# Kernel tuning notes

Measured on AMD Instinct MI355X. Metric: run time of the kernel, lower is better.

## Reference

```python
import jax, jax.numpy as jnp
import numpy as np

B, T, D = 8, 2048, 1024
FF = 4 * D
EPS = 1e-5


def setup_inputs() -> dict:
    key = jax.random.key(0)
    ks = jax.random.split(key, 20)
    rn = lambda k, s, sc=0.02: (jax.random.normal(k, s, jnp.float32) * sc)
    return {
        "x": jax.random.normal(ks[0], (B, T, D), jnp.float32),
        "ln1_g": jnp.ones((D,), jnp.float32),
        "ln1_b": jnp.zeros((D,), jnp.float32),
        "ln2_g": jnp.ones((D,), jnp.float32),
        "ln2_b": jnp.zeros((D,), jnp.float32),
        # time-mixing lerp coefficients in [0,1]
        "tm_mix_k": jax.random.uniform(ks[1], (D,), jnp.float32),
        "tm_mix_v": jax.random.uniform(ks[2], (D,), jnp.float32),
        "tm_mix_r": jax.random.uniform(ks[3], (D,), jnp.float32),
        # per-channel decay (log-log space, w = -exp(time_decay)) and first-token bonus
        "time_decay": rn(ks[4], (D,), 1.0),
        "time_first": rn(ks[5], (D,), 0.5),
        "wk": rn(ks[6], (D, D)),
        "wv": rn(ks[7], (D, D)),
        "wr": rn(ks[8], (D, D)),
        "wo": rn(ks[9], (D, D)),
        "cm_mix_k": jax.random.uniform(ks[10], (D,), jnp.float32),
        "cm_mix_r": jax.random.uniform(ks[11], (D,), jnp.float32),
        "cwk": rn(ks[12], (D, FF)),
        "cwv": rn(ks[13], (FF, D)),
        "cwr": rn(ks[14], (D, D)),
    }


def layer_norm(x, g, b):
    mu = jnp.mean(x, axis=-1, keepdims=True)
    var = jnp.var(x, axis=-1, keepdims=True)
    return (x - mu) * jax.lax.rsqrt(var + EPS) * g + b


def token_shift(x):
    # x[:, t-1] with zeros at t=0 (fresh state)
    return jnp.pad(x, ((0, 0), (1, 0), (0, 0)))[:, :-1]


def wkv_scan(k, v, time_decay, time_first):
    """Numerically-stable RWKV-4 WKV linear recurrence. k,v: [B,T,D]."""
    w = -jnp.exp(time_decay)  # [D], negative log-decay per step
    u = time_first

    def step(carry, kv):
        aa, bb, pp = carry  # each [B, D]
        kt, vt = kv
        ww = u + kt
        p = jnp.maximum(pp, ww)
        e1 = jnp.exp(pp - p)
        e2 = jnp.exp(ww - p)
        out = (e1 * aa + e2 * vt) / (e1 * bb + e2)
        ww2 = pp + w
        p2 = jnp.maximum(ww2, kt)
        e1b = jnp.exp(ww2 - p2)
        e2b = jnp.exp(kt - p2)
        return (e1b * aa + e2b * vt, e1b * bb + e2b, p2), out

    z = jnp.zeros((k.shape[0], k.shape[2]), k.dtype)
    init = (z, z, jnp.full_like(z, -1e38))
    _, outs = jax.lax.scan(step, init, (jnp.moveaxis(k, 1, 0), jnp.moveaxis(v, 1, 0)))
    return jnp.moveaxis(outs, 0, 1)  # [B,T,D]


def reference(x, ln1_g, ln1_b, ln2_g, ln2_b,
              tm_mix_k, tm_mix_v, tm_mix_r, time_decay, time_first,
              wk, wv, wr, wo, cm_mix_k, cm_mix_r, cwk, cwv, cwr):
    # --- Time mixing (pre-LN residual) ---
    h = layer_norm(x, ln1_g, ln1_b)
    hx = token_shift(h)
    k = jnp.einsum("btd,de->bte", h * tm_mix_k + hx * (1.0 - tm_mix_k), wk)
    v = jnp.einsum("btd,de->bte", h * tm_mix_v + hx * (1.0 - tm_mix_v), wv)
    r = jax.nn.sigmoid(jnp.einsum("btd,de->bte", h * tm_mix_r + hx * (1.0 - tm_mix_r), wr))
    wkv = wkv_scan(k, v, time_decay, time_first)
    x = x + jnp.einsum("btd,de->bte", r * wkv, wo)

    # --- Channel mixing (pre-LN residual) ---
    h = layer_norm(x, ln2_g, ln2_b)
    hx = token_shift(h)
    kk = jnp.einsum("btd,df->btf", h * cm_mix_k + hx * (1.0 - cm_mix_k), cwk)
    kk = jnp.square(jax.nn.relu(kk))  # [B,T,4D]
    rr = jax.nn.sigmoid(jnp.einsum("btd,de->bte", h * cm_mix_r + hx * (1.0 - cm_mix_r), cwr))
    x = x + rr * jnp.einsum("btf,fd->btd", kk, cwv)
    return x
```

## Files before the change

kernel.cpp:

```cpp
#include <hip/hip_runtime.h>

typedef unsigned short u16;
typedef float f32x4 __attribute__((ext_vector_type(4)));
typedef __bf16 bf16x8 __attribute__((ext_vector_type(8)));
typedef u16 u16x8 __attribute__((ext_vector_type(8)));
typedef u16 u16x4 __attribute__((ext_vector_type(4)));

static constexpr int D  = 1024;
static constexpr int T  = 2048;
static constexpr int NB = 8;
static constexpr int M  = NB * T;
static constexpr int FF = 4096;
static constexpr int NCH = 32;
static constexpr int CL  = T / NCH;

__device__ __forceinline__ u16 f2bf(float f) {
  unsigned u = __builtin_bit_cast(unsigned, f);
  return (u16)((u + 0x7fffu + ((u >> 16) & 1u)) >> 16);
}
__device__ __forceinline__ float bf2f(u16 s) {
  return __builtin_bit_cast(float, (unsigned)s << 16);
}

__device__ __forceinline__ void gload16(const u16* g, u16* l) {
  __builtin_amdgcn_global_load_lds(
      (const __attribute__((address_space(1))) void*)g,
      (__attribute__((address_space(3))) void*)l, 16, 0, 0);
}

__global__ __launch_bounds__(256) void ln_kernel(const float* __restrict__ x,
                                                 const float* __restrict__ g,
                                                 const float* __restrict__ b,
                                                 u16* __restrict__ h) {
  __shared__ float red[8];
  const int m = blockIdx.x;
  const int tid = threadIdx.x;
  const float* xr = x + (size_t)m * D;
  f32x4 v = *(const f32x4*)&xr[tid * 4];
  float s  = v[0] + v[1] + v[2] + v[3];
  float s2 = v[0]*v[0] + v[1]*v[1] + v[2]*v[2] + v[3]*v[3];
  #pragma unroll
  for (int o = 32; o > 0; o >>= 1) { s += __shfl_down(s, o); s2 += __shfl_down(s2, o); }
  if ((tid & 63) == 0) { red[tid >> 6] = s; red[4 + (tid >> 6)] = s2; }
  __syncthreads();
  s  = red[0] + red[1] + red[2] + red[3];
  s2 = red[4] + red[5] + red[6] + red[7];
  const float mu = s * (1.0f / D);
  const float rs = rsqrtf(s2 * (1.0f / D) - mu * mu + 1e-5f);
  u16x4 o4;
  #pragma unroll
  for (int i = 0; i < 4; ++i) {
    int d = tid * 4 + i;
    o4[i] = f2bf((v[i] - mu) * rs * g[d] + b[d]);
  }
  *(u16x4*)&h[(size_t)m * D + tid * 4] = o4;
}

__global__ __launch_bounds__(256) void mix3_kernel(const u16* __restrict__ h,
    const float* __restrict__ mk, const float* __restrict__ mv, const float* __restrict__ mr,
    u16* __restrict__ xk, u16* __restrict__ xv, u16* __restrict__ xr) {
  const int m = blockIdx.x;
  const int tid = threadIdx.x;
  const size_t base = (size_t)m * D + tid * 4;
  u16x4 hv = *(const u16x4*)&h[base];
  u16x4 hp = {0, 0, 0, 0};
  if ((m % T) != 0) hp = *(const u16x4*)&h[base - D];
  u16x4 ok, ov, orr;
  #pragma unroll
  for (int i = 0; i < 4; ++i) {
    int d = tid * 4 + i;
    float hc = bf2f(hv[i]), hx = bf2f(hp[i]);
    float a;
    a = mk[d]; ok[i]  = f2bf(hc * a + hx * (1.0f - a));
    a = mv[d]; ov[i]  = f2bf(hc * a + hx * (1.0f - a));
    a = mr[d]; orr[i] = f2bf(hc * a + hx * (1.0f - a));
  }
  *(u16x4*)&xk[base] = ok;
  *(u16x4*)&xv[base] = ov;
  *(u16x4*)&xr[base] = orr;
}

__global__ __launch_bounds__(256) void mix2_kernel(const u16* __restrict__ h,
    const float* __restrict__ mk, const float* __restrict__ mr,
    u16* __restrict__ xk, u16* __restrict__ xr) {
  const int m = blockIdx.x;
  const int tid = threadIdx.x;
  const size_t base = (size_t)m * D + tid * 4;
  u16x4 hv = *(const u16x4*)&h[base];
  u16x4 hp = {0, 0, 0, 0};
  if ((m % T) != 0) hp = *(const u16x4*)&h[base - D];
  u16x4 ok, orr;
  #pragma unroll
  for (int i = 0; i < 4; ++i) {
    int d = tid * 4 + i;
    float hc = bf2f(hv[i]), hx = bf2f(hp[i]);
    float a;
    a = mk[d]; ok[i]  = f2bf(hc * a + hx * (1.0f - a));
    a = mr[d]; orr[i] = f2bf(hc * a + hx * (1.0f - a));
  }
  *(u16x4*)&xk[base] = ok;
  *(u16x4*)&xr[base] = orr;
}

__global__ __launch_bounds__(256) void transpose_bf16_kernel(const float* __restrict__ in,
                                                             u16* __restrict__ out,
                                                             int K_, int N_) {
  __shared__ u16 t[32][33];
  const int k0 = blockIdx.x * 32, n0 = blockIdx.y * 32;
  const int r = threadIdx.x >> 5, c = threadIdx.x & 31;
  #pragma unroll
  for (int p = 0; p < 4; ++p)
    t[r + p * 8][c] = f2bf(in[(size_t)(k0 + r + p * 8) * N_ + n0 + c]);
  __syncthreads();
  #pragma unroll
  for (int p = 0; p < 4; ++p)
    out[(size_t)(n0 + r + p * 8) * K_ + k0 + c] = t[c][r + p * 8];
}

__global__ __launch_bounds__(256) void wkv_phase1(const float* __restrict__ K_,
                                                  const u16* __restrict__ V_,
                                                  const float* __restrict__ td,
                                                  float* __restrict__ aggA,
                                                  float* __restrict__ aggB,
                                                  float* __restrict__ aggP) {
  const int gid = blockIdx.x * 256 + threadIdx.x;
  const int d = gid & (D - 1);
  const int c = (gid >> 10) & (NCH - 1);
  const int b = gid >> 15;
  const float w = -expf(td[d]);
  float a = 0.0f, bb = 0.0f, p = -1e38f;
  size_t idx = ((size_t)b * T + (size_t)c * CL) * D + d;
  for (int t = 0; t < CL; ++t, idx += D) {
    const float kt = K_[idx];
    const float vt = bf2f(V_[idx]);
    const float wp = p + w;
    const float pn = fmaxf(wp, kt);
    const float e1 = expf(wp - pn), e2 = expf(kt - pn);
    a  = e1 * a  + e2 * vt;
    bb = e1 * bb + e2;
    p  = pn;
  }
  aggA[gid] = a; aggB[gid] = bb; aggP[gid] = p;
}

__global__ __launch_bounds__(256) void wkv_phase2(const float* __restrict__ td,
                                                  const float* __restrict__ aggA,
                                                  const float* __restrict__ aggB,
                                                  const float* __restrict__ aggP,
                                                  float* __restrict__ incA,
                                                  float* __restrict__ incB,
                                                  float* __restrict__ incP) {
  const int gid = blockIdx.x * 256 + threadIdx.x;
  const int d = gid & (D - 1);
  const int b = gid >> 10;
  const float cw = -expf(td[d]) * (float)CL;
  float a = 0.0f, bb = 0.0f, p = -1e38f;
  for (int c = 0; c < NCH; ++c) {
    const int i = (b * NCH + c) * D + d;
    incA[i] = a; incB[i] = bb; incP[i] = p;
    const float pd = p + cw;
    const float pc = aggP[i];
    const float pn = fmaxf(pd, pc);
    const float e1 = expf(pd - pn), e2 = expf(pc - pn);
    a  = e1 * a  + e2 * aggA[i];
    bb = e1 * bb + e2 * aggB[i];
    p  = pn;
  }
}

__global__ __launch_bounds__(256) void wkv_phase3(const float* __restrict__ K_,
                                                  const u16* __restrict__ V_,
                                                  const u16* __restrict__ R_,
                                                  const float* __restrict__ td,
                                                  const float* __restrict__ tf,
                                                  const float* __restrict__ incA,
                                                  const float* __restrict__ incB,
                                                  const float* __restrict__ incP,
                                                  u16* __restrict__ a2) {
  const int gid = blockIdx.x * 256 + threadIdx.x;
  const int d = gid & (D - 1);
  const int c = (gid >> 10) & (NCH - 1);
  const int b = gid >> 15;
  const float w = -expf(td[d]);
  const float u = tf[d];
  float aa = incA[gid], bb = incB[gid], pp = incP[gid];
  size_t idx = ((size_t)b * T + (size_t)c * CL) * D + d;
  for (int t = 0; t < CL; ++t, idx += D) {
    const float kt = K_[idx];
    const float vt = bf2f(V_[idx]);
    const float rt = bf2f(R_[idx]);
    const float ww = u + kt;
    const float p  = fmaxf(pp, ww);
    const float e1 = expf(pp - p), e2 = expf(ww - p);
    const float o  = (e1 * aa + e2 * vt) / (e1 * bb + e2);
    a2[idx] = f2bf(rt * o);
    const float ww2 = pp + w;
    const float p2  = fmaxf(ww2, kt);
    const float e1b = expf(ww2 - p2), e2b = expf(kt - p2);
    aa = e1b * aa + e2b * vt;
    bb = e1b * bb + e2b;
    pp = p2;
  }
}

template <int EPI>
__global__ __launch_bounds__(512, 2) void gemm8(const u16* __restrict__ A,
                                                const u16* __restrict__ Bt,
                                                int N, int K,
                                                float* __restrict__ outf,
                                                u16* __restrict__ outh,
                                                const float* __restrict__ auxf,
                                                const u16* __restrict__ auxh,
                                                float* __restrict__ dst) {
  __shared__ u16 sm[65536];
  const int gx = gridDim.x, gy = gridDim.y;
  const int fid = blockIdx.y * gx + blockIdx.x;
  const int xcd = fid & 7, sl = fid >> 3;
  const int m0 = (xcd * (gx >> 3) + sl / gy) * 256;
  const int n0 = (sl % gy) * 256;

  const int tid = threadIdx.x;
  const int w = tid >> 6, l = tid & 63;
  const int wm = w >> 2, wn = w & 3;
  const int lr = l >> 3, ls = l & 7;
  const int NT = K >> 6;
  f32x4 acc[8][4] = {};

  const u16* gA = A + (size_t)(m0 + w * 8 + lr) * K + (ls ^ lr) * 8;
  const u16* gB = Bt + (size_t)(n0 + w * 8 + lr) * K + (ls ^ lr) * 8;

  auto stA = [&](int j, int r) {
    gload16(gA + ((size_t)r * 64) * K + (size_t)j * 64,
            &sm[(j & 1) * 16384 + (r * 64 + w * 8) * 64]);
  };
  auto stB = [&](int j, int r) {
    gload16(gB + ((size_t)r * 64) * K + (size_t)j * 64,
            &sm[32768 + (j & 1) * 16384 + (r * 64 + w * 8) * 64]);
  };

  u16x8 bF[4][2], aA[2][2], aB[2][2];

  auto ldB8 = [&](const u16* sB) {
    #pragma unroll
    for (int ni = 0; ni < 4; ++ni)
      #pragma unroll
      for (int ks = 0; ks < 2; ++ks) {
        const int rb = wn * 64 + ni * 16 + (l & 15);
        const int rs = ks * 4 + (l >> 4);
        bF[ni][ks] = *(const u16x8*)&sB[rb * 64 + ((rs ^ (rb & 7)) * 8)];
      }
  };

#define LDA(q, dstf, sAp)                                                   \
  _Pragma("unroll") for (int mi = 0; mi < 2; ++mi)                          \
    _Pragma("unroll") for (int ks = 0; ks < 2; ++ks) {                      \
      const int ra = wm * 128 + (q) * 32 + mi * 16 + (l & 15);              \
      const int rs = ks * 4 + (l >> 4);                                     \
      dstf[mi][ks] = *(const u16x8*)&sAp[ra * 64 + ((rs ^ (ra & 7)) * 8)];  \
    }

#define MFMA16(Q, srcf)                                                     \
  __builtin_amdgcn_s_setprio(1);                                            \
  _Pragma("unroll") for (int ks = 0; ks < 2; ++ks)                          \
    _Pragma("unroll") for (int mi = 0; mi < 2; ++mi)                        \
      _Pragma("unroll") for (int ni = 0; ni < 4; ++ni)                      \
        acc[(Q) * 2 + mi][ni] = __builtin_amdgcn_mfma_f32_16x16x32_bf16(    \
            __builtin_bit_cast(bf16x8, srcf[mi][ks]),                       \
            __builtin_bit_cast(bf16x8, bF[ni][ks]),                         \
            acc[(Q) * 2 + mi][ni], 0, 0, 0);                                \
  __builtin_amdgcn_s_setprio(0);

  stB(0, 0); stB(0, 1); stB(0, 2); stB(0, 3);
  stA(0, 0); stA(0, 1); stA(0, 2); stA(0, 3);
  if (1 < NT) {
    stB(1, 0); stB(1, 1); stB(1, 2); stB(1, 3);
    stA(1, 0); stA(1, 1); stA(1, 2); stA(1, 3);
    asm volatile("s_waitcnt vmcnt(8)" ::: "memory");
  } else {
    asm volatile("s_waitcnt vmcnt(0)" ::: "memory");
  }
  __builtin_amdgcn_s_barrier();
  ldB8(&sm[32768]);
  LDA(0, aA, (&sm[0]));

  for (int k = 0; k < NT; ++k) {
    const u16* sA  = &sm[(k & 1) * 16384];
    const u16* sAn = &sm[((k + 1) & 1) * 16384];
    const u16* sBn = &sm[32768 + ((k + 1) & 1) * 16384];
    LDA(1, aB, sA);
    if (k + 2 < NT) { stB(k + 2, 0); stB(k + 2, 1); }
    MFMA16(0, aA);
    __builtin_amdgcn_s_barrier();
    LDA(2, aA, sA);
    if (k + 2 < NT) { stB(k + 2, 2); stB(k + 2, 3); }
    MFMA16(1, aB);
    __builtin_amdgcn_s_barrier();
    LDA(3, aB, sA);
    if (k + 2 < NT) { stA(k + 2, 0); stA(k + 2, 2); }
    MFMA16(2, aA);
    __builtin_amdgcn_s_barrier();
    if (k + 2 < NT) {
      stA(k + 2, 1); stA(k + 2, 3);
      asm volatile("s_waitcnt vmcnt(8)" ::: "memory");
    } else if (k + 1 < NT) {
      asm volatile("s_waitcnt vmcnt(0)" ::: "memory");
    }
    __builtin_amdgcn_s_barrier();
    MFMA16(3, aB);
    if (k + 1 < NT) { ldB8(sBn); LDA(0, aA, sAn); }
    __builtin_amdgcn_s_barrier();
  }
#undef LDA
#undef MFMA16

  const int cl = l & 15, rh = l >> 4;
  #pragma unroll
  for (int mi = 0; mi < 8; ++mi) {
    #pragma unroll
    for (int ni = 0; ni < 4; ++ni) {
      const int gn = n0 + wn * 64 + ni * 16 + cl;
      #pragma unroll
      for (int j = 0; j < 4; ++j) {
        const int gm = m0 + wm * 128 + mi * 16 + rh * 4 + j;
        const float c = acc[mi][ni][j];
        const size_t o = (size_t)gm * N + gn;
        if (EPI == 0) outf[o] = c;
        else if (EPI == 1) outh[o] = f2bf(1.0f / (1.0f + expf(-c)));
        else if (EPI == 2) outf[o] = auxf[o] + c;
        else if (EPI == 3) { const float t = c > 0.0f ? c : 0.0f; outh[o] = f2bf(t * t); }
        else if (EPI == 4) dst[o] += bf2f(auxh[o]) * c;
        else if (EPI == 5) outh[o] = f2bf(c);
      }
    }
  }
}

extern "C" void kernel_launch(void* const* d_in, const int* in_sizes, int n_in,
                              void* d_out, int out_size, void* d_ws, size_t ws_size,
                              hipStream_t stream) {
  (void)in_sizes; (void)n_in; (void)out_size;
  const float* x      = (const float*)d_in[0];
  const float* ln1_g  = (const float*)d_in[1];
  const float* ln1_b  = (const float*)d_in[2];
  const float* ln2_g  = (const float*)d_in[3];
  const float* ln2_b  = (const float*)d_in[4];
  const float* tm_k   = (const float*)d_in[5];
  const float* tm_v   = (const float*)d_in[6];
  const float* tm_r   = (const float*)d_in[7];
  const float* tdec   = (const float*)d_in[8];
  const float* tfir   = (const float*)d_in[9];
  const float* wk     = (const float*)d_in[10];
  const float* wv     = (const float*)d_in[11];
  const float* wr     = (const float*)d_in[12];
  const float* wo     = (const float*)d_in[13];
  const float* cm_k   = (const float*)d_in[14];
  const float* cm_r   = (const float*)d_in[15];
  const float* cwk    = (const float*)d_in[16];
  const float* cwv    = (const float*)d_in[17];
  const float* cwr    = (const float*)d_in[18];
  float* out = (float*)d_out;

  const size_t MB = 1024 * 1024;
  if (ws_size < 218 * MB) return;

  char* w = (char*)d_ws;
  u16*   h    = (u16*)(w);
  u16*   b32  = (u16*)(w + 32 * MB);
  u16*   b64  = (u16*)(w + 64 * MB);
  u16*   b96  = (u16*)(w + 96 * MB);
  float* Kf   = (float*)(w + 128 * MB);
  u16*   KK   = (u16*)(w + 64 * MB);
  u16*   wkT  = (u16*)(w + 192 * MB);
  u16*   wvT  = (u16*)(w + 194 * MB);
  u16*   wrT  = (u16*)(w + 196 * MB);
  u16*   woT  = (u16*)(w + 198 * MB);
  u16*   cwkT = (u16*)(w + 200 * MB);
  u16*   cwvT = (u16*)(w + 208 * MB);
  u16*   cwrT = (u16*)(w + 216 * MB);
  float* aggA = (float*)(w + 96 * MB);
  float* aggB = (float*)(w + 97 * MB);
  float* aggP = (float*)(w + 98 * MB);
  float* incA = (float*)(w + 99 * MB);
  float* incB = (float*)(w + 100 * MB);
  float* incP = (float*)(w + 101 * MB);

  transpose_bf16_kernel<<<dim3(D / 32, D / 32), 256, 0, stream>>>(wk, wkT, D, D);
  transpose_bf16_kernel<<<dim3(D / 32, D / 32), 256, 0, stream>>>(wv, wvT, D, D);
  transpose_bf16_kernel<<<dim3(D / 32, D / 32), 256, 0, stream>>>(wr, wrT, D, D);
  transpose_bf16_kernel<<<dim3(D / 32, D / 32), 256, 0, stream>>>(wo, woT, D, D);
  transpose_bf16_kernel<<<dim3(D / 32, FF / 32), 256, 0, stream>>>(cwk, cwkT, D, FF);
  transpose_bf16_kernel<<<dim3(FF / 32, D / 32), 256, 0, stream>>>(cwv, cwvT, FF, D);
  transpose_bf16_kernel<<<dim3(D / 32, D / 32), 256, 0, stream>>>(cwr, cwrT, D, D);

  ln_kernel<<<M, 256, 0, stream>>>(x, ln1_g, ln1_b, h);
  mix3_kernel<<<M, 256, 0, stream>>>(h, tm_k, tm_v, tm_r, b32, b64, b96);

  dim3 gD(M / 256, D / 256);
  gemm8<0><<<gD, 512, 0, stream>>>(b32, wkT, D, D, Kf, nullptr, nullptr, nullptr, nullptr);
  gemm8<5><<<gD, 512, 0, stream>>>(b64, wvT, D, D, nullptr, b32, nullptr, nullptr, nullptr);
  gemm8<1><<<gD, 512, 0, stream>>>(b96, wrT, D, D, nullptr, h, nullptr, nullptr, nullptr);

  wkv_phase1<<<(NB * NCH * D) / 256, 256, 0, stream>>>(Kf, b32, tdec, aggA, aggB, aggP);
  wkv_phase2<<<(NB * D) / 256, 256, 0, stream>>>(tdec, aggA, aggB, aggP, incA, incB, incP);
  wkv_phase3<<<(NB * NCH * D) / 256, 256, 0, stream>>>(Kf, b32, h, tdec, tfir,
                                                       incA, incB, incP, b64);

  gemm8<2><<<gD, 512, 0, stream>>>(b64, woT, D, D, out, nullptr, x, nullptr, nullptr);

  ln_kernel<<<M, 256, 0, stream>>>(out, ln2_g, ln2_b, h);
  mix2_kernel<<<M, 256, 0, stream>>>(h, cm_k, cm_r, b32, b64);

  gemm8<1><<<gD, 512, 0, stream>>>(b64, cwrT, D, D, nullptr, h, nullptr, nullptr, nullptr);

  dim3 gF(M / 256, FF / 256);
  gemm8<3><<<gF, 512, 0, stream>>>(b32, cwkT, FF, D, nullptr, KK, nullptr, nullptr, nullptr);

  dim3 gO(M / 256, D / 256);
  gemm8<4><<<gO, 512, 0, stream>>>(KK, cwvT, D, FF, nullptr, nullptr, nullptr, h, out);
}
```

Before: 719.7 us.

## Replace ping-pong A fragments with single buffer and explicit LDS fences in GEMM loop

The GEMM main loop drops the two alternating A register fragment sets (aA/aB) for a single fragment array. Each quarter now loads its A slice from LDS, fences with lgkmcnt(0) and a sched_barrier, then issues its MFMAs. The B fragments are loaded at the start of each iteration instead of prefetched at the end of the previous one, and extra block barriers are added. This lowers register pressure and makes the schedule explicit, but gives up the overlap of LDS reads with MFMA work and adds synchronization.

```diff
diff --git a/kernel.cpp b/kernel.cpp
--- a/kernel.cpp
+++ b/kernel.cpp
@@ -238,7 +238,7 @@
             &sm[32768 + (j & 1) * 16384 + (r * 64 + w * 8) * 64]);
   };
 
-  u16x8 bF[4][2], aA[2][2], aB[2][2];
+  u16x8 bF[4][2], aF[2][2];
 
   auto ldB8 = [&](const u16* sB) {
     #pragma unroll
@@ -251,24 +251,28 @@
       }
   };
 
-#define LDA(q, dstf, sAp)                                                   \
+#define LDA(q, sAp)                                                         \
   _Pragma("unroll") for (int mi = 0; mi < 2; ++mi)                          \
     _Pragma("unroll") for (int ks = 0; ks < 2; ++ks) {                      \
       const int ra = wm * 128 + (q) * 32 + mi * 16 + (l & 15);              \
       const int rs = ks * 4 + (l >> 4);                                     \
-      dstf[mi][ks] = *(const u16x8*)&sAp[ra * 64 + ((rs ^ (ra & 7)) * 8)];  \
+      aF[mi][ks] = *(const u16x8*)&sAp[ra * 64 + ((rs ^ (ra & 7)) * 8)];    \
     }
 
-#define MFMA16(Q, srcf)                                                     \
+#define MFMA16(Q)                                                           \
   __builtin_amdgcn_s_setprio(1);                                            \
   _Pragma("unroll") for (int ks = 0; ks < 2; ++ks)                          \
     _Pragma("unroll") for (int mi = 0; mi < 2; ++mi)                        \
       _Pragma("unroll") for (int ni = 0; ni < 4; ++ni)                      \
         acc[(Q) * 2 + mi][ni] = __builtin_amdgcn_mfma_f32_16x16x32_bf16(    \
-            __builtin_bit_cast(bf16x8, srcf[mi][ks]),                       \
+            __builtin_bit_cast(bf16x8, aF[mi][ks]),                         \
             __builtin_bit_cast(bf16x8, bF[ni][ks]),                         \
             acc[(Q) * 2 + mi][ni], 0, 0, 0);                                \
   __builtin_amdgcn_s_setprio(0);
+
+#define LGKM0_FENCE                                                         \
+  asm volatile("s_waitcnt lgkmcnt(0)" ::: "memory");                        \
+  __builtin_amdgcn_sched_barrier(0);
 
   stB(0, 0); stB(0, 1); stB(0, 2); stB(0, 3);
   stA(0, 0); stA(0, 1); stA(0, 2); stA(0, 3);
@@ -280,38 +284,45 @@
     asm volatile("s_waitcnt vmcnt(0)" ::: "memory");
   }
   __builtin_amdgcn_s_barrier();
-  ldB8(&sm[32768]);
-  LDA(0, aA, (&sm[0]));
 
   for (int k = 0; k < NT; ++k) {
-    const u16* sA  = &sm[(k & 1) * 16384];
-    const u16* sAn = &sm[((k + 1) & 1) * 16384];
-    const u16* sBn = &sm[32768 + ((k + 1) & 1) * 16384];
-    LDA(1, aB, sA);
-    if (k + 2 < NT) { stB(k + 2, 0); stB(k + 2, 1); }
-    MFMA16(0, aA);
-    __builtin_amdgcn_s_barrier();
-    LDA(2, aA, sA);
-    if (k + 2 < NT) { stB(k + 2, 2); stB(k + 2, 3); }
-    MFMA16(1, aB);
-    __builtin_amdgcn_s_barrier();
-    LDA(3, aB, sA);
-    if (k + 2 < NT) { stA(k + 2, 0); stA(k + 2, 2); }
-    MFMA16(2, aA);
-    __builtin_amdgcn_s_barrier();
-    if (k + 2 < NT) {
+    const u16* sA = &sm[(k & 1) * 16384];
+    const u16* sB = &sm[32768 + (k & 1) * 16384];
+    const bool s2 = (k + 2 < NT);
+    ldB8(sB);
+    LDA(0, sA);
+    asm volatile("s_waitcnt lgkmcnt(8)" ::: "memory");
+    __builtin_amdgcn_s_barrier();
+    LGKM0_FENCE
+    MFMA16(0);
+    __builtin_amdgcn_s_barrier();
+    LDA(1, sA);
+    if (s2) { stB(k + 2, 0); stB(k + 2, 1); }
+    __builtin_amdgcn_s_barrier();
+    LGKM0_FENCE
+    MFMA16(1);
+    __builtin_amdgcn_s_barrier();
+    LDA(2, sA);
+    if (s2) { stB(k + 2, 2); stB(k + 2, 3); stA(k + 2, 0); stA(k + 2, 2); }
+    __builtin_amdgcn_s_barrier();
+    LGKM0_FENCE
+    MFMA16(2);
+    __builtin_amdgcn_s_barrier();
+    LDA(3, sA);
+    __builtin_amdgcn_s_barrier();
+    LGKM0_FENCE
+    if (s2) {
       stA(k + 2, 1); stA(k + 2, 3);
-      asm volatile("s_waitcnt vmcnt(8)" ::: "memory");
+      asm volatile("s_waitcnt vmcnt(6)" ::: "memory");
     } else if (k + 1 < NT) {
       asm volatile("s_waitcnt vmcnt(0)" ::: "memory");
     }
-    __builtin_amdgcn_s_barrier();
-    MFMA16(3, aB);
-    if (k + 1 < NT) { ldB8(sBn); LDA(0, aA, sAn); }
+    MFMA16(3);
     __builtin_amdgcn_s_barrier();
   }
 #undef LDA
 #undef MFMA16
+#undef LGKM0_FENCE
 
   const int cl = l & 15, rh = l >> 4;
   #pragma unroll
```

After: 726.5 us. About the same (+1.0%).
